# Kernel tuning notes

Measured on AMD Instinct MI355X. Metric: run time of the kernel, lower is better.

## Reference

```python
import jax, jax.numpy as jnp
import numpy as np

B, CPD, T = 32, 64, 1024
IN_DIM, HID, WIN = 256, 512, 1024
SCALE = 0.02  # make_initializer(0.02)


def setup_inputs() -> dict:
    key = jax.random.key(0)
    k1, k2, k3, k4, k5 = jax.random.split(key, 5)
    return {
        "control": jax.random.normal(k1, (B, CPD, T), dtype=jnp.float32),
        "proj": jax.random.normal(k2, (CPD, IN_DIM), dtype=jnp.float32) * 0.01,
        "W_ih": jax.random.normal(k3, (HID, IN_DIM), dtype=jnp.float32) * SCALE,
        "W_hh": jax.random.normal(k4, (HID, HID), dtype=jnp.float32) * SCALE,
        "W_out": jax.random.normal(k5, (WIN, HID), dtype=jnp.float32) * SCALE,
    }


def reference(control, proj, W_ih, W_hh, W_out):
    # control: (b, c, t) -> (b, t, c) @ (c, i) -> (b, t, i)
    x = jnp.einsum('bct,ci->bti', control, proj)
    # precompute input-to-hidden contribution for all timesteps: (b, t, h)
    xw = jnp.einsum('bti,hi->bth', x, W_ih)

    Whh_T = W_hh.T  # (h, h)

    def step(h, xt):  # h: (b, h), xt: (b, h)
        h_new = jnp.tanh(xt + h @ Whh_T)
        return h_new, h_new

    b = control.shape[0]
    h0 = jnp.zeros((b, W_hh.shape[0]), dtype=control.dtype)
    _, hs = jax.lax.scan(step, h0, jnp.swapaxes(xw, 0, 1))  # (t, b, h)
    hs = jnp.swapaxes(hs, 0, 1)  # (b, t, h)

    # out_proj (no bias): (b, t, h) @ (h, w) -> (b, t, w)
    out = jnp.einsum('bth,wh->btw', hs, W_out)
    return jnp.sin(out.reshape(b, 1, -1))  # (b, 1, t*w)
```

## Files before the change

kernel.cpp:

```cpp
#include <hip/hip_runtime.h>

#define BATCH   32
#define CPD     64
#define TSTEPS  1024
#define IN_DIM  256
#define HID     512
#define WIN     1024

typedef _Float16 half2_t __attribute__((ext_vector_type(2)));
typedef _Float16 f16x8   __attribute__((ext_vector_type(8)));
typedef float    f32x4   __attribute__((ext_vector_type(4)));

#define TAG_SALT 0x5A5A0000u

__device__ __forceinline__ float tanh_fast(float x) {
    float e = __expf(2.0f * x);
    return 1.0f - 2.0f / (e + 1.0f);
}

__global__ __launch_bounds__(512) void k_a1(const float* __restrict__ proj,
                                            const float* __restrict__ W_ih,
                                            float* __restrict__ M_t) {
    __shared__ float p[IN_DIM];
    int c = blockIdx.x;
    if (threadIdx.x < IN_DIM) p[threadIdx.x] = proj[c * IN_DIM + threadIdx.x];
    __syncthreads();
    int h = threadIdx.x;
    const float4* wr = (const float4*)(W_ih + (size_t)h * IN_DIM);
    float acc = 0.f;
#pragma unroll
    for (int i = 0; i < IN_DIM / 4; ++i) {
        float4 v = wr[i];
        acc += v.x * p[4*i] + v.y * p[4*i+1] + v.z * p[4*i+2] + v.w * p[4*i+3];
    }
    M_t[(size_t)h * CPD + c] = acc;
}

__global__ __launch_bounds__(256) void k_cvt(const float* __restrict__ src,
                                             _Float16* __restrict__ dst) {
    int i = (blockIdx.x * 256 + threadIdx.x) * 4;
    float4 v = *(const float4*)(src + i);
    dst[i+0] = (_Float16)v.x; dst[i+1] = (_Float16)v.y;
    dst[i+2] = (_Float16)v.z; dst[i+3] = (_Float16)v.w;
}

__global__ __launch_bounds__(512) void k_a2(const float* __restrict__ control,
                                            const float* __restrict__ M_t,
                                            float* __restrict__ xw) {
    __shared__ float ctl[CPD][68];
    int b  = blockIdx.x >> 4;
    int t0 = (blockIdx.x & 15) * 64;
    int tid = threadIdx.x;

    const float* gb = control + (size_t)b * CPD * TSTEPS + t0;
#pragma unroll
    for (int i = 0; i < 2; ++i) {
        int flat4 = tid * 2 + i;
        int c = flat4 >> 4, t4 = (flat4 & 15) * 4;
        float4 v = *(const float4*)(gb + (size_t)c * TSTEPS + t4);
        *(float4*)&ctl[c][t4] = v;
    }
    int h = tid;
    float mrow[CPD];
    const float4* mp = (const float4*)(M_t + (size_t)h * CPD);
#pragma unroll
    for (int i = 0; i < CPD / 4; ++i) {
        float4 v = mp[i];
        mrow[4*i] = v.x; mrow[4*i+1] = v.y; mrow[4*i+2] = v.z; mrow[4*i+3] = v.w;
    }
    __syncthreads();

    float* xo = xw + ((size_t)b * TSTEPS + t0) * HID + h;
#pragma unroll
    for (int half = 0; half < 2; ++half) {
        float acc[32];
#pragma unroll
        for (int q = 0; q < 32; ++q) acc[q] = 0.f;
#pragma unroll
        for (int c = 0; c < CPD; ++c) {
            float m = mrow[c];
#pragma unroll
            for (int q = 0; q < 8; ++q) {
                float4 v = *(const float4*)&ctl[c][half * 32 + q * 4];
                acc[q*4+0] += v.x * m; acc[q*4+1] += v.y * m;
                acc[q*4+2] += v.z * m; acc[q*4+3] += v.w * m;
            }
        }
#pragma unroll
        for (int tt = 0; tt < 32; ++tt)
            xo[(size_t)(half * 32 + tt) * HID] = acc[tt];
    }
}

__device__ __forceinline__ void publish(unsigned long long* p, unsigned int tag, float v) {
    unsigned long long pk = ((unsigned long long)tag << 32) | (unsigned long long)__float_as_uint(v);
    __hip_atomic_store(p, pk, __ATOMIC_RELAXED, __HIP_MEMORY_SCOPE_AGENT);
}
__device__ __forceinline__ float poll(unsigned long long* p, unsigned int want) {
    unsigned long long v;
    do {
        v = __hip_atomic_load(p, __ATOMIC_RELAXED, __HIP_MEMORY_SCOPE_AGENT);
    } while ((unsigned int)(v >> 32) != want);
    return __uint_as_float((unsigned int)v);
}

__global__ __launch_bounds__(256, 1) void k_scan(const float* __restrict__ W_hh,
                                                 const float* __restrict__ xw,
                                                 unsigned long long* __restrict__ hbuf,
                                                 _Float16* __restrict__ hs) {
    int bid = blockIdx.x;
    int b = bid & 31, chunk = bid >> 5;
    int r0 = chunk * 64;
    int tid = threadIdx.x;
    int l = tid & 63, c = tid >> 6;

    half2_t w[64];
    const float2* wr = (const float2*)(W_hh + (size_t)(r0 + l) * HID + c * 128);
#pragma unroll
    for (int j = 0; j < 64; ++j) {
        float2 f = wr[j];
        half2_t hv = {(_Float16)f.x, (_Float16)f.y};
        w[j] = hv;
    }

    __shared__ half2_t hlds[256];
    __shared__ float   part[4][64];

    unsigned long long* hb0 = hbuf + (size_t)b * HID;
    unsigned long long* hb1 = hbuf + (size_t)BATCH * HID + (size_t)b * HID;
    const float* xwb = xw + (size_t)b * TSTEPS * HID;
    _Float16* hsb = hs + (size_t)b * TSTEPS * HID;

    float xw_next = 0.f;
    if (tid < 64) {
        int r = r0 + tid;
        float hv = tanh_fast(xwb[r]);
        hsb[r] = (_Float16)hv;
        publish(hb1 + r, TAG_SALT + 1u, hv);
        xw_next = xwb[HID + r];
    }

#pragma unroll 1
    for (int t = 2; t <= TSTEPS; ++t) {
        unsigned long long* rdbuf = ((t - 1) & 1) ? hb1 : hb0;
        unsigned long long* wrbuf = (t & 1) ? hb1 : hb0;
        unsigned int want = TAG_SALT + (unsigned int)(t - 1);
        float v0 = poll(rdbuf + 2 * tid, want);
        float v1 = poll(rdbuf + 2 * tid + 1, want);
        half2_t hv = {(_Float16)v0, (_Float16)v1};
        hlds[tid] = hv;
        __syncthreads();

        const half2_t* hp = hlds + c * 64;
        float a0 = 0.f, a1 = 0.f, a2 = 0.f, a3 = 0.f;
#pragma unroll
        for (int q = 0; q < 16; ++q) {
            half2_t h0 = hp[4*q], h1 = hp[4*q+1], h2 = hp[4*q+2], h3 = hp[4*q+3];
            a0 = __builtin_amdgcn_fdot2(w[4*q+0], h0, a0, false);
            a1 = __builtin_amdgcn_fdot2(w[4*q+1], h1, a1, false);
            a2 = __builtin_amdgcn_fdot2(w[4*q+2], h2, a2, false);
            a3 = __builtin_amdgcn_fdot2(w[4*q+3], h3, a3, false);
        }
        part[c][l] = (a0 + a1) + (a2 + a3);
        __syncthreads();

        if (tid < 64) {
            int r = r0 + tid;
            float s = part[0][tid] + part[1][tid] + part[2][tid] + part[3][tid] + xw_next;
            float hv2 = tanh_fast(s);
            hsb[(size_t)(t - 1) * HID + r] = (_Float16)hv2;
            publish(wrbuf + r, TAG_SALT + (unsigned int)t, hv2);
            if (t < TSTEPS) xw_next = xwb[(size_t)t * HID + r];
        }
    }
}

__global__ void k_outgemm(const _Float16* __restrict__ hs,
                          const _Float16* __restrict__ Wo,
                          float* __restrict__ out) {
    __shared__ _Float16 Ap[128][40];
    __shared__ _Float16 Bp[128][40];
    int tid = threadIdx.x;
    int r0 = blockIdx.x * 128;
    int c0 = blockIdx.y * 128;
    int wid = tid >> 6, l = tid & 63;
    int wr = (wid >> 1) * 64, wc = (wid & 1) * 64;
    int lrow = tid & 127, lhalf = (tid >> 7) * 16;
    int fr = l & 15, kg = (l >> 4) * 8;

    f32x4 acc[4][4];
#pragma unroll
    for (int m = 0; m < 4; ++m)
#pragma unroll
        for (int n = 0; n < 4; ++n) acc[m][n] = (f32x4){0.f, 0.f, 0.f, 0.f};

    for (int k0 = 0; k0 < HID; k0 += 32) {
        const uint4* ga = (const uint4*)(hs + (size_t)(r0 + lrow) * HID + k0 + lhalf);
        uint4 a0 = ga[0], a1 = ga[1];
        const uint4* gbp = (const uint4*)(Wo + (size_t)(c0 + lrow) * HID + k0 + lhalf);
        uint4 b0 = gbp[0], b1 = gbp[1];
        __syncthreads();
        *(uint4*)&Ap[lrow][lhalf] = a0; *(uint4*)&Ap[lrow][lhalf + 8] = a1;
        *(uint4*)&Bp[lrow][lhalf] = b0; *(uint4*)&Bp[lrow][lhalf + 8] = b1;
        __syncthreads();

        f16x8 af[4], bf[4];
#pragma unroll
        for (int m = 0; m < 4; ++m) af[m] = *(const f16x8*)&Ap[wr + m * 16 + fr][kg];
#pragma unroll
        for (int n = 0; n < 4; ++n) bf[n] = *(const f16x8*)&Bp[wc + n * 16 + fr][kg];
#pragma unroll
        for (int m = 0; m < 4; ++m)
#pragma unroll
            for (int n = 0; n < 4; ++n)
                acc[m][n] = __builtin_amdgcn_mfma_f32_16x16x32_f16(af[m], bf[n], acc[m][n], 0, 0, 0);
    }

    int fq = l >> 4;
#pragma unroll
    for (int m = 0; m < 4; ++m)
#pragma unroll
        for (int n = 0; n < 4; ++n)
#pragma unroll
            for (int q = 0; q < 4; ++q) {
                int row = r0 + wr + m * 16 + fq * 4 + q;
                int col = c0 + wc + n * 16 + fr;
                out[(size_t)row * WIN + col] = __sinf(acc[m][n][q]);
            }
}

extern "C" void kernel_launch(void* const* d_in, const int* in_sizes, int n_in,
                              void* d_out, int out_size, void* d_ws, size_t ws_size,
                              hipStream_t stream) {
    const float* control = (const float*)d_in[0];
    const float* proj    = (const float*)d_in[1];
    const float* W_ih    = (const float*)d_in[2];
    const float* W_hh    = (const float*)d_in[3];
    const float* W_out   = (const float*)d_in[4];
    float* out = (float*)d_out;

    const size_t XW_B   = (size_t)BATCH * TSTEPS * HID * 4;
    const size_t MT_B   = (size_t)HID * CPD * 4;
    const size_t HBUF_B = 2ull * BATCH * HID * 8;
    const size_t HS_B   = (size_t)BATCH * TSTEPS * HID * 2;
    const size_t WO_B   = (size_t)WIN * HID * 2;
    if (ws_size < XW_B + MT_B + HBUF_B + HS_B + WO_B) return;

    char* ws = (char*)d_ws;
    float* xw = (float*)ws;                          ws += XW_B;
    float* M_t = (float*)ws;                         ws += MT_B;
    unsigned long long* hbuf = (unsigned long long*)ws; ws += HBUF_B;
    _Float16* hs = (_Float16*)ws;                    ws += HS_B;
    _Float16* Wo = (_Float16*)ws;

    k_a1<<<CPD, 512, 0, stream>>>(proj, W_ih, M_t);
    k_cvt<<<512, 256, 0, stream>>>(W_out, Wo);
    k_a2<<<BATCH * 16, 512, 0, stream>>>(control, M_t, xw);
    k_scan<<<256, 256, 0, stream>>>(W_hh, xw, hbuf, hs);
    k_outgemm<<<dim3(256, 8), 256, 0, stream>>>(hs, Wo, out);
}
```

Measured before the change: 1.647 ms.

## Run each batch's RNN scan in one 1024-thread block, drop cross-block polling

The recurrent scan moves from 8 cooperating blocks per batch element, which exchanged hidden state through tagged atomic stores and polling in global memory, to a single 1024-thread block per batch element. Each thread keeps 8 rows by 32 columns of W_hh in registers as fp16, reads the fp16 hidden state from a double-buffered shared array, and reduces partial dot products with a butterfly of lane shuffles. Each step then needs only one block barrier instead of device-scope atomics. The trade-off is that only 32 CUs run the scan, and each thread carries a large register footprint. The output GEMM grid is also transposed so that consecutive blocks share the same hs rows.

Result: slower. 3.527 ms (+114.2%).

```diff
diff --git a/kernel.cpp b/kernel.cpp
--- a/kernel.cpp
+++ b/kernel.cpp
@@ -10,8 +10,6 @@
 typedef _Float16 half2_t __attribute__((ext_vector_type(2)));
 typedef _Float16 f16x8   __attribute__((ext_vector_type(8)));
 typedef float    f32x4   __attribute__((ext_vector_type(4)));
-
-#define TAG_SALT 0x5A5A0000u
 
 __device__ __forceinline__ float tanh_fast(float x) {
     float e = __expf(2.0f * x);
@@ -92,86 +90,101 @@
     }
 }
 
-__device__ __forceinline__ void publish(unsigned long long* p, unsigned int tag, float v) {
-    unsigned long long pk = ((unsigned long long)tag << 32) | (unsigned long long)__float_as_uint(v);
-    __hip_atomic_store(p, pk, __ATOMIC_RELAXED, __HIP_MEMORY_SCOPE_AGENT);
-}
-__device__ __forceinline__ float poll(unsigned long long* p, unsigned int want) {
-    unsigned long long v;
-    do {
-        v = __hip_atomic_load(p, __ATOMIC_RELAXED, __HIP_MEMORY_SCOPE_AGENT);
-    } while ((unsigned int)(v >> 32) != want);
-    return __uint_as_float((unsigned int)v);
-}
-
-__global__ __launch_bounds__(256, 1) void k_scan(const float* __restrict__ W_hh,
-                                                 const float* __restrict__ xw,
-                                                 unsigned long long* __restrict__ hbuf,
-                                                 _Float16* __restrict__ hs) {
-    int bid = blockIdx.x;
-    int b = bid & 31, chunk = bid >> 5;
-    int r0 = chunk * 64;
-    int tid = threadIdx.x;
-    int l = tid & 63, c = tid >> 6;
-
-    half2_t w[64];
-    const float2* wr = (const float2*)(W_hh + (size_t)(r0 + l) * HID + c * 128);
-#pragma unroll
-    for (int j = 0; j < 64; ++j) {
-        float2 f = wr[j];
-        half2_t hv = {(_Float16)f.x, (_Float16)f.y};
-        w[j] = hv;
-    }
-
-    __shared__ half2_t hlds[256];
-    __shared__ float   part[4][64];
-
-    unsigned long long* hb0 = hbuf + (size_t)b * HID;
-    unsigned long long* hb1 = hbuf + (size_t)BATCH * HID + (size_t)b * HID;
+__global__ __launch_bounds__(1024) void k_scan(const float* __restrict__ W_hh,
+                                               const float* __restrict__ xw,
+                                               _Float16* __restrict__ hs) {
+    const int b    = blockIdx.x;
+    const int tid  = threadIdx.x;
+    const int cs   = tid & 15;
+    const int rb   = tid >> 4;
+    const int lane = tid & 63;
+    const int w    = tid >> 6;
+
+    half2_t wreg[8][16];
+#pragma unroll
+    for (int j = 0; j < 8; ++j) {
+        const float* src = W_hh + (size_t)(rb * 8 + j) * HID + cs * 32;
+#pragma unroll
+        for (int q = 0; q < 16; q += 2) {
+            float4 f = *(const float4*)(src + 2 * q);
+            wreg[j][q]     = (half2_t){(_Float16)f.x, (_Float16)f.y};
+            wreg[j][q + 1] = (half2_t){(_Float16)f.z, (_Float16)f.w};
+        }
+    }
+
+    __shared__ __align__(16) _Float16 hb[2][16 * 40];
+
+    const int myrow  = w * 32 + ((lane >> 4) << 3) + (lane & 7);
+    const bool writer = !(lane & 8);
+    const bool b0 = lane & 1, b1 = lane & 2, b2 = lane & 4;
+
     const float* xwb = xw + (size_t)b * TSTEPS * HID;
-    _Float16* hsb = hs + (size_t)b * TSTEPS * HID;
-
-    float xw_next = 0.f;
-    if (tid < 64) {
-        int r = r0 + tid;
-        float hv = tanh_fast(xwb[r]);
-        hsb[r] = (_Float16)hv;
-        publish(hb1 + r, TAG_SALT + 1u, hv);
-        xw_next = xwb[HID + r];
-    }
+    _Float16*    hsb = hs + (size_t)b * TSTEPS * HID;
+
+    {
+        float h0 = tanh_fast(xwb[myrow]);
+        _Float16 hf = (_Float16)h0;
+        if (writer) {
+            hb[0][w * 40 + (myrow & 31)] = hf;
+            hsb[myrow] = hf;
+        }
+    }
+    __syncthreads();
 
 #pragma unroll 1
-    for (int t = 2; t <= TSTEPS; ++t) {
-        unsigned long long* rdbuf = ((t - 1) & 1) ? hb1 : hb0;
-        unsigned long long* wrbuf = (t & 1) ? hb1 : hb0;
-        unsigned int want = TAG_SALT + (unsigned int)(t - 1);
-        float v0 = poll(rdbuf + 2 * tid, want);
-        float v1 = poll(rdbuf + 2 * tid + 1, want);
-        half2_t hv = {(_Float16)v0, (_Float16)v1};
-        hlds[tid] = hv;
+    for (int t = 1; t < TSTEPS; ++t) {
+        float xwv = xwb[(size_t)t * HID + myrow];
+
+        const _Float16* rp = &hb[(t + 1) & 1][cs * 40];
+        f16x8 hv0 = *(const f16x8*)(rp);
+        f16x8 hv1 = *(const f16x8*)(rp + 8);
+        f16x8 hv2 = *(const f16x8*)(rp + 16);
+        f16x8 hv3 = *(const f16x8*)(rp + 24);
+        half2_t h2[16];
+#pragma unroll
+        for (int q = 0; q < 4; ++q) {
+            h2[q]      = (half2_t){hv0[2 * q], hv0[2 * q + 1]};
+            h2[4 + q]  = (half2_t){hv1[2 * q], hv1[2 * q + 1]};
+            h2[8 + q]  = (half2_t){hv2[2 * q], hv2[2 * q + 1]};
+            h2[12 + q] = (half2_t){hv3[2 * q], hv3[2 * q + 1]};
+        }
+
+        float a[8];
+#pragma unroll
+        for (int j = 0; j < 8; ++j) a[j] = 0.f;
+#pragma unroll
+        for (int q = 0; q < 16; ++q) {
+#pragma unroll
+            for (int j = 0; j < 8; ++j)
+                a[j] = __builtin_amdgcn_fdot2(wreg[j][q], h2[q], a[j], false);
+        }
+
+#pragma unroll
+        for (int j = 0; j < 4; ++j) {
+            float snd = b0 ? a[2 * j] : a[2 * j + 1];
+            float kp  = b0 ? a[2 * j + 1] : a[2 * j];
+            a[j] = kp + __shfl_xor(snd, 1, 64);
+        }
+#pragma unroll
+        for (int j = 0; j < 2; ++j) {
+            float snd = b1 ? a[2 * j] : a[2 * j + 1];
+            float kp  = b1 ? a[2 * j + 1] : a[2 * j];
+            a[j] = kp + __shfl_xor(snd, 2, 64);
+        }
+        {
+            float snd = b2 ? a[0] : a[1];
+            float kp  = b2 ? a[1] : a[0];
+            a[0] = kp + __shfl_xor(snd, 4, 64);
+        }
+        a[0] += __shfl_xor(a[0], 8, 64);
+
+        float hval = tanh_fast(a[0] + xwv);
+        _Float16 hfv = (_Float16)hval;
+        if (writer) {
+            hb[t & 1][w * 40 + (myrow & 31)] = hfv;
+            hsb[(size_t)t * HID + myrow] = hfv;
+        }
         __syncthreads();
-
-        const half2_t* hp = hlds + c * 64;
-        float a0 = 0.f, a1 = 0.f, a2 = 0.f, a3 = 0.f;
-#pragma unroll
-        for (int q = 0; q < 16; ++q) {
-            half2_t h0 = hp[4*q], h1 = hp[4*q+1], h2 = hp[4*q+2], h3 = hp[4*q+3];
-            a0 = __builtin_amdgcn_fdot2(w[4*q+0], h0, a0, false);
-            a1 = __builtin_amdgcn_fdot2(w[4*q+1], h1, a1, false);
-            a2 = __builtin_amdgcn_fdot2(w[4*q+2], h2, a2, false);
-            a3 = __builtin_amdgcn_fdot2(w[4*q+3], h3, a3, false);
-        }
-        part[c][l] = (a0 + a1) + (a2 + a3);
-        __syncthreads();
-
-        if (tid < 64) {
-            int r = r0 + tid;
-            float s = part[0][tid] + part[1][tid] + part[2][tid] + part[3][tid] + xw_next;
-            float hv2 = tanh_fast(s);
-            hsb[(size_t)(t - 1) * HID + r] = (_Float16)hv2;
-            publish(wrbuf + r, TAG_SALT + (unsigned int)t, hv2);
-            if (t < TSTEPS) xw_next = xwb[(size_t)t * HID + r];
-        }
     }
 }
 
@@ -181,8 +194,8 @@
     __shared__ _Float16 Ap[128][40];
     __shared__ _Float16 Bp[128][40];
     int tid = threadIdx.x;
-    int r0 = blockIdx.x * 128;
-    int c0 = blockIdx.y * 128;
+    int r0 = blockIdx.y * 128;
+    int c0 = blockIdx.x * 128;
     int wid = tid >> 6, l = tid & 63;
     int wr = (wid >> 1) * 64, wc = (wid & 1) * 64;
     int lrow = tid & 127, lhalf = (tid >> 7) * 16;
@@ -241,21 +254,19 @@
 
     const size_t XW_B   = (size_t)BATCH * TSTEPS * HID * 4;
     const size_t MT_B   = (size_t)HID * CPD * 4;
-    const size_t HBUF_B = 2ull * BATCH * HID * 8;
     const size_t HS_B   = (size_t)BATCH * TSTEPS * HID * 2;
     const size_t WO_B   = (size_t)WIN * HID * 2;
-    if (ws_size < XW_B + MT_B + HBUF_B + HS_B + WO_B) return;
+    if (ws_size < XW_B + MT_B + HS_B + WO_B) return;
 
     char* ws = (char*)d_ws;
     float* xw = (float*)ws;                          ws += XW_B;
     float* M_t = (float*)ws;                         ws += MT_B;
-    unsigned long long* hbuf = (unsigned long long*)ws; ws += HBUF_B;
     _Float16* hs = (_Float16*)ws;                    ws += HS_B;
     _Float16* Wo = (_Float16*)ws;
 
     k_a1<<<CPD, 512, 0, stream>>>(proj, W_ih, M_t);
     k_cvt<<<512, 256, 0, stream>>>(W_out, Wo);
     k_a2<<<BATCH * 16, 512, 0, stream>>>(control, M_t, xw);
-    k_scan<<<256, 256, 0, stream>>>(W_hh, xw, hbuf, hs);
-    k_outgemm<<<dim3(256, 8), 256, 0, stream>>>(hs, Wo, out);
-}
+    k_scan<<<BATCH, 1024, 0, stream>>>(W_hh, xw, hs);
+    k_outgemm<<<dim3(8, 256), 256, 0, stream>>>(hs, Wo, out);
+}
```
